# Kernel optimization log

Hardware: AMD Instinct MI355X
Metric: run time of the kernel (lower is better)

The kernel has to match this reference:

```python
import jax, jax.numpy as jnp
import numpy as np

EMBED_DIM = 1024
NUM_HEADS = 16
HEAD_DIM = EMBED_DIM // NUM_HEADS


def setup_inputs() -> dict:
    key = jax.random.key(0)
    ks = jax.random.split(key, 6)
    B, S, D = 2, 2048, EMBED_DIM
    scale = 1.0 / np.sqrt(D)
    return {
        "inputs": jax.random.normal(ks[0], (B, S, D), dtype=jnp.float32),
        "Wq": jax.random.normal(ks[1], (D, D), dtype=jnp.float32) * scale,
        "Wk": jax.random.normal(ks[2], (D, D), dtype=jnp.float32) * scale,
        "Wv": jax.random.normal(ks[3], (D, D), dtype=jnp.float32) * scale,
        "Wo": jax.random.normal(ks[4], (D, D), dtype=jnp.float32) * scale,
        "bo": jnp.zeros((D,), dtype=jnp.float32),
    }


def reference(inputs, Wq, Wk, Wv, Wo, bo):
    B, S, D = inputs.shape
    H, P = NUM_HEADS, HEAD_DIM
    # torch Linear: x @ W.T ; weights stored [out, in]
    q = inputs @ Wq.T
    k = inputs @ Wk.T
    v = inputs @ Wv.T
    # separate heads: [B, S, H, P] -> [B, H, S, P]
    q = q.reshape(B, S, H, P).transpose(0, 2, 1, 3)
    k = k.reshape(B, S, H, P).transpose(0, 2, 1, 3)
    v = v.reshape(B, S, H, P).transpose(0, 2, 1, 3)
    # scaled dot-product attention; scale = 1/sqrt(P + 1e-9)
    scale = 1.0 / jnp.sqrt(jnp.float32(P) + 1e-9)
    scores = jnp.einsum("bhsp,bhtp->bhst", q, k) * scale
    weights = jax.nn.softmax(scores, axis=-1)
    attn = jnp.einsum("bhst,bhtp->bhsp", weights, v)
    # merge heads -> [B, S, D]
    concat = attn.transpose(0, 2, 1, 3).reshape(B, S, D)
    return concat @ Wo.T + bo
```

## Files before the change

### kernel.cpp

```cpp
#include <hip/hip_runtime.h>
#include <hip/hip_bf16.h>

typedef __bf16 bf16;
typedef __bf16 bf16x4 __attribute__((ext_vector_type(4)));
typedef __bf16 bf16x8 __attribute__((ext_vector_type(8)));
typedef short  s16x4  __attribute__((ext_vector_type(4)));
typedef float  f32x4  __attribute__((ext_vector_type(4)));

#define QSCALE 0.18033688011112042f

__device__ __forceinline__ void load16_lds(const bf16* g, bf16* l) {
    __builtin_amdgcn_global_load_lds(
        (const __attribute__((address_space(1))) unsigned int*)g,
        (__attribute__((address_space(3))) unsigned int*)l, 16, 0, 0);
}

__global__ void cvt_f32_bf16(
    const float* __restrict__ s0, const float* __restrict__ s1,
    const float* __restrict__ s2, const float* __restrict__ s3,
    const float* __restrict__ s4,
    bf16* __restrict__ d0, bf16* __restrict__ d1, bf16* __restrict__ d2,
    bf16* __restrict__ d3, bf16* __restrict__ d4)
{
    const float* s; bf16* d; int nblk;
    switch (blockIdx.y) {
        case 0:  s = s0; d = d0; nblk = 2048; break;
        case 1:  s = s1; d = d1; nblk = 512;  break;
        case 2:  s = s2; d = d2; nblk = 512;  break;
        case 3:  s = s3; d = d3; nblk = 512;  break;
        default: s = s4; d = d4; nblk = 512;  break;
    }
    if ((int)blockIdx.x >= nblk) return;
    int idx = blockIdx.x * 256 + threadIdx.x;
    float4 a = ((const float4*)s)[idx * 2];
    float4 b = ((const float4*)s)[idx * 2 + 1];
    bf16x8 o;
    o[0] = (bf16)a.x; o[1] = (bf16)a.y; o[2] = (bf16)a.z; o[3] = (bf16)a.w;
    o[4] = (bf16)b.x; o[5] = (bf16)b.y; o[6] = (bf16)b.z; o[7] = (bf16)b.w;
    *(bf16x8*)&d[idx * 8] = o;
}

__global__ __launch_bounds__(256, 2) void qkv_gemm(
    const bf16* __restrict__ A,
    const bf16* __restrict__ Wq, const bf16* __restrict__ Wk,
    const bf16* __restrict__ Wv,
    bf16* __restrict__ qbuf, bf16* __restrict__ kbuf, bf16* __restrict__ vT)
{
    __shared__ bf16 sA[128 * 32];
    __shared__ bf16 sB[128 * 32];

    const int which = blockIdx.x >> 3;
    const int n0    = (blockIdx.x & 7) * 128;
    const int m0    = blockIdx.y * 128;
    const bf16* B   = (which == 0) ? Wq : (which == 1) ? Wk : Wv;

    const int tid  = threadIdx.x;
    const int lane = tid & 63;
    const int w    = tid >> 6;
    const int wr   = w >> 1, wc = w & 1;
    const int r    = lane & 15;
    const int qd   = lane >> 4;

    f32x4 acc[4][4];
    const f32x4 zero4 = {0.f, 0.f, 0.f, 0.f};
#pragma unroll
    for (int mi = 0; mi < 4; ++mi)
#pragma unroll
        for (int ni = 0; ni < 4; ++ni) acc[mi][ni] = zero4;

    for (int kt = 0; kt < 32; ++kt) {
        const bf16* gA = A + (size_t)m0 * 1024 + kt * 32;
        const bf16* gB = B + (size_t)n0 * 1024 + kt * 32;
        __syncthreads();
#pragma unroll
        for (int j = 0; j < 2; ++j) {
            int task = j * 256 + tid;
            int row  = task >> 2, ch = task & 3;
            int ldsb = (j * 256 + w * 64) * 8;
            load16_lds(gA + (size_t)row * 1024 + ch * 8, &sA[ldsb]);
            load16_lds(gB + (size_t)row * 1024 + ch * 8, &sB[ldsb]);
        }
        __syncthreads();

        bf16x8 af[4], bfr[4];
#pragma unroll
        for (int mi = 0; mi < 4; ++mi)
            af[mi] = *(const bf16x8*)&sA[(wr * 64 + mi * 16 + r) * 32 + qd * 8];
#pragma unroll
        for (int ni = 0; ni < 4; ++ni)
            bfr[ni] = *(const bf16x8*)&sB[(wc * 64 + ni * 16 + r) * 32 + qd * 8];
#pragma unroll
        for (int mi = 0; mi < 4; ++mi)
#pragma unroll
            for (int ni = 0; ni < 4; ++ni)
                acc[mi][ni] = __builtin_amdgcn_mfma_f32_16x16x32_bf16(
                    af[mi], bfr[ni], acc[mi][ni], 0, 0, 0);
    }

    const float scale = (which == 0) ? QSCALE : 1.0f;
#pragma unroll
    for (int mi = 0; mi < 4; ++mi)
#pragma unroll
        for (int ni = 0; ni < 4; ++ni)
#pragma unroll
            for (int i = 0; i < 4; ++i) {
                int row = m0 + wr * 64 + mi * 16 + qd * 4 + i;
                int col = n0 + wc * 64 + ni * 16 + r;
                float v = acc[mi][ni][i] * scale;
                if (which == 0) {
                    qbuf[(size_t)row * 1024 + col] = (bf16)v;
                } else if (which == 1) {
                    kbuf[(size_t)row * 1024 + col] = (bf16)v;
                } else {
                    vT[((size_t)((row >> 11) * 1024 + col)) * 2048 + (row & 2047)] = (bf16)v;
                }
            }
}

__global__ __launch_bounds__(256, 2) void out_gemm(
    const bf16* __restrict__ A, const bf16* __restrict__ B,
    float* __restrict__ C, const float* __restrict__ bias)
{
    __shared__ bf16 sA[128 * 32];
    __shared__ bf16 sB[64 * 32];

    const int tid  = threadIdx.x;
    const int lane = tid & 63;
    const int w    = tid >> 6;
    const int wr   = w >> 1, wc = w & 1;
    const int r    = lane & 15;
    const int qd   = lane >> 4;
    const int m0   = blockIdx.y * 128;
    const int n0   = blockIdx.x * 64;

    f32x4 acc[4][2];
    const f32x4 zero4 = {0.f, 0.f, 0.f, 0.f};
#pragma unroll
    for (int mi = 0; mi < 4; ++mi)
#pragma unroll
        for (int ni = 0; ni < 2; ++ni) acc[mi][ni] = zero4;

    for (int kt = 0; kt < 32; ++kt) {
        const bf16* gA = A + (size_t)m0 * 1024 + kt * 32;
        const bf16* gB = B + (size_t)n0 * 1024 + kt * 32;
        __syncthreads();
#pragma unroll
        for (int j = 0; j < 2; ++j) {
            int task = j * 256 + tid;
            int row  = task >> 2, ch = task & 3;
            int ldsb = (j * 256 + w * 64) * 8;
            load16_lds(gA + (size_t)row * 1024 + ch * 8, &sA[ldsb]);
        }
        {
            int row = tid >> 2, ch = tid & 3;
            int ldsb = (w * 64) * 8;
            load16_lds(gB + (size_t)row * 1024 + ch * 8, &sB[ldsb]);
        }
        __syncthreads();

        bf16x8 af[4], bfr[2];
#pragma unroll
        for (int mi = 0; mi < 4; ++mi)
            af[mi] = *(const bf16x8*)&sA[(wr * 64 + mi * 16 + r) * 32 + qd * 8];
#pragma unroll
        for (int ni = 0; ni < 2; ++ni)
            bfr[ni] = *(const bf16x8*)&sB[(wc * 32 + ni * 16 + r) * 32 + qd * 8];
#pragma unroll
        for (int mi = 0; mi < 4; ++mi)
#pragma unroll
            for (int ni = 0; ni < 2; ++ni)
                acc[mi][ni] = __builtin_amdgcn_mfma_f32_16x16x32_bf16(
                    af[mi], bfr[ni], acc[mi][ni], 0, 0, 0);
    }

#pragma unroll
    for (int mi = 0; mi < 4; ++mi)
#pragma unroll
        for (int ni = 0; ni < 2; ++ni)
#pragma unroll
            for (int i = 0; i < 4; ++i) {
                int row = m0 + wr * 64 + mi * 16 + qd * 4 + i;
                int col = n0 + wc * 32 + ni * 16 + r;
                C[(size_t)row * 1024 + col] = acc[mi][ni][i] + bias[col];
            }
}

__global__ __launch_bounds__(256, 2) void attn_kernel(
    const bf16* __restrict__ qbuf, const bf16* __restrict__ kbuf,
    const bf16* __restrict__ vT, bf16* __restrict__ concat)
{
    __shared__ bf16 sKV[4 * 64 * 72];

    const int tid  = threadIdx.x;
    const int lane = tid & 63;
    const int w    = tid >> 6;
    const int r    = lane & 15;
    const int qd   = lane >> 4;
    const int qt   = blockIdx.x;
    const int bh   = blockIdx.y;
    const int b    = bh >> 4, h = bh & 15;
    const int qrow0 = b * 2048 + qt * 128;
    const size_t vbase = (size_t)bh * 64 * 2048;

    const s16x4 ones4 = {(short)0x3F80, (short)0x3F80, (short)0x3F80, (short)0x3F80};

    int krow[2], kch[2];
#pragma unroll
    for (int t = 0; t < 2; ++t) {
        int flat = t * 256 + tid;
        krow[t] = flat >> 3; kch[t] = flat & 7;
    }

    bf16x8 aq[2][2];
#pragma unroll
    for (int mi = 0; mi < 2; ++mi)
#pragma unroll
        for (int ks = 0; ks < 2; ++ks)
            aq[mi][ks] = *(const bf16x8*)&qbuf[
                (size_t)(qrow0 + w * 32 + mi * 16 + r) * 1024 + h * 64 + ks * 32 + qd * 8];

    f32x4 acc_o[2][4], acc_l[2];
    const f32x4 zero4 = {0.f, 0.f, 0.f, 0.f};
#pragma unroll
    for (int mi = 0; mi < 2; ++mi) {
        acc_l[mi] = zero4;
#pragma unroll
        for (int pj = 0; pj < 4; ++pj) acc_o[mi][pj] = zero4;
    }

    bf16x8 rk[2], rv[2];
#pragma unroll
    for (int t = 0; t < 2; ++t) {
        rk[t] = *(const bf16x8*)&kbuf[(size_t)(b * 2048 + krow[t]) * 1024 + h * 64 + kch[t] * 8];
        rv[t] = *(const bf16x8*)&vT[vbase + (size_t)krow[t] * 2048 + kch[t] * 8];
    }
#pragma unroll
    for (int t = 0; t < 2; ++t) {
        *(bf16x8*)&sKV[0 * 4608 + krow[t] * 72 + kch[t] * 8] = rk[t];
        *(bf16x8*)&sKV[1 * 4608 + krow[t] * 72 + kch[t] * 8] = rv[t];
    }
#pragma unroll
    for (int t = 0; t < 2; ++t) {
        rk[t] = *(const bf16x8*)&kbuf[(size_t)(b * 2048 + 64 + krow[t]) * 1024 + h * 64 + kch[t] * 8];
        rv[t] = *(const bf16x8*)&vT[vbase + (size_t)krow[t] * 2048 + 64 + kch[t] * 8];
    }
    __syncthreads();

    for (int tt = 0; tt < 32; ++tt) {
        {
            int st = (tt + 1) & 1;
#pragma unroll
            for (int t = 0; t < 2; ++t) {
                *(bf16x8*)&sKV[(2 * st + 0) * 4608 + krow[t] * 72 + kch[t] * 8] = rk[t];
                *(bf16x8*)&sKV[(2 * st + 1) * 4608 + krow[t] * 72 + kch[t] * 8] = rv[t];
            }
        }
        {
            int nxt = (tt + 2 < 32) ? tt + 2 : 31;
#pragma unroll
            for (int t = 0; t < 2; ++t) {
                rk[t] = *(const bf16x8*)&kbuf[(size_t)(b * 2048 + nxt * 64 + krow[t]) * 1024 + h * 64 + kch[t] * 8];
                rv[t] = *(const bf16x8*)&vT[vbase + (size_t)krow[t] * 2048 + nxt * 64 + kch[t] * 8];
            }
        }
        const bf16* sK = &sKV[(2 * (tt & 1) + 0) * 4608];
        const bf16* sV = &sKV[(2 * (tt & 1) + 1) * 4608];

        f32x4 accs[2][4];
#pragma unroll
        for (int mi = 0; mi < 2; ++mi)
#pragma unroll
            for (int ni = 0; ni < 4; ++ni) accs[mi][ni] = zero4;
#pragma unroll
        for (int ks = 0; ks < 2; ++ks)
#pragma unroll
            for (int ni = 0; ni < 4; ++ni) {
                bf16x8 ak = *(const bf16x8*)&sK[(ni * 16 + r) * 72 + ks * 32 + qd * 8];
#pragma unroll
                for (int mi = 0; mi < 2; ++mi)
                    accs[mi][ni] = __builtin_amdgcn_mfma_f32_16x16x32_bf16(
                        ak, aq[mi][ks], accs[mi][ni], 0, 0, 0);
            }

        s16x4 pfrag[2][4];
#pragma unroll
        for (int mi = 0; mi < 2; ++mi)
#pragma unroll
            for (int ni = 0; ni < 4; ++ni) {
                bf16x4 pv;
#pragma unroll
                for (int i = 0; i < 4; ++i) pv[i] = (bf16)exp2f(accs[mi][ni][i]);
                pfrag[mi][ni] = __builtin_bit_cast(s16x4, pv);
            }

#pragma unroll
        for (int ni = 0; ni < 4; ++ni) {
#pragma unroll
            for (int pj = 0; pj < 4; ++pj) {
                bf16x4 av = *(const bf16x4*)&sV[(pj * 16 + r) * 72 + ni * 16 + qd * 4];
                s16x4  avs = __builtin_bit_cast(s16x4, av);
#pragma unroll
                for (int mi = 0; mi < 2; ++mi)
                    acc_o[mi][pj] = __builtin_amdgcn_mfma_f32_16x16x16bf16_1k(
                        avs, pfrag[mi][ni], acc_o[mi][pj], 0, 0, 0);
            }
#pragma unroll
            for (int mi = 0; mi < 2; ++mi)
                acc_l[mi] = __builtin_amdgcn_mfma_f32_16x16x16bf16_1k(
                    ones4, pfrag[mi][ni], acc_l[mi], 0, 0, 0);
        }

        __syncthreads();
    }

    bf16* scratch = sKV;
#pragma unroll
    for (int mi = 0; mi < 2; ++mi) {
        float inv = 1.0f / acc_l[mi][0];
        int qloc  = w * 32 + mi * 16 + r;
#pragma unroll
        for (int pj = 0; pj < 4; ++pj)
#pragma unroll
            for (int i = 0; i < 4; ++i)
                scratch[qloc * 72 + pj * 16 + qd * 4 + i] =
                    (bf16)(acc_o[mi][pj][i] * inv);
    }
    __syncthreads();
    {
        int row  = tid >> 1;
        int half = tid & 1;
#pragma unroll
        for (int c = 0; c < 4; ++c) {
            bf16x8 v = *(const bf16x8*)&scratch[row * 72 + half * 32 + c * 8];
            *(bf16x8*)&concat[(size_t)(qrow0 + row) * 1024 + h * 64 + half * 32 + c * 8] = v;
        }
    }
}

extern "C" void kernel_launch(void* const* d_in, const int* in_sizes, int n_in,
                              void* d_out, int out_size, void* d_ws, size_t ws_size,
                              hipStream_t stream)
{
    const float* x  = (const float*)d_in[0];
    const float* Wq = (const float*)d_in[1];
    const float* Wk = (const float*)d_in[2];
    const float* Wv = (const float*)d_in[3];
    const float* Wo = (const float*)d_in[4];
    const float* bo = (const float*)d_in[5];
    float* out = (float*)d_out;

    char* ws = (char*)d_ws;
    bf16* xb     = (bf16*)(ws);
    bf16* Wqb    = (bf16*)(ws + (8u  << 20));
    bf16* Wkb    = (bf16*)(ws + (10u << 20));
    bf16* Wvb    = (bf16*)(ws + (12u << 20));
    bf16* Wob    = (bf16*)(ws + (14u << 20));
    bf16* qbuf   = (bf16*)(ws + (16u << 20));
    bf16* kbuf   = (bf16*)(ws + (24u << 20));
    bf16* vT     = (bf16*)(ws + (32u << 20));
    bf16* concat = (bf16*)(ws + (40u << 20));

    hipLaunchKernelGGL(cvt_f32_bf16, dim3(2048, 5), dim3(256), 0, stream,
                       x, Wq, Wk, Wv, Wo, xb, Wqb, Wkb, Wvb, Wob);
    hipLaunchKernelGGL(qkv_gemm, dim3(24, 32), dim3(256), 0, stream,
                       xb, Wqb, Wkb, Wvb, qbuf, kbuf, vT);
    hipLaunchKernelGGL(attn_kernel, dim3(16, 32), dim3(256), 0, stream,
                       qbuf, kbuf, vT, concat);
    hipLaunchKernelGGL(out_gemm, dim3(16, 32), dim3(256), 0, stream,
                       concat, Wob, out, bo);
}
```

Measured before the change: 206.3 us.

## Split attention KV sequence across two wave groups and vectorize V-transpose stores

The attention kernel now runs 512 threads per block as two groups of four waves. Each group handles alternating 64-key tiles for the same 128 queries, using its own double-buffered LDS region, and the partial O and row-sum accumulators are merged through LDS at the end. This doubles the waves working per query tile to raise latency hiding and occupancy, at the cost of more LDS, a reduction step and a larger register budget per block. Separately, the QKV GEMM epilogue writes the transposed V as packed 4-element bf16 vectors instead of scalar stores.

```diff
diff --git a/kernel.cpp b/kernel.cpp
--- a/kernel.cpp
+++ b/kernel.cpp
@@ -101,20 +101,21 @@
 #pragma unroll
     for (int mi = 0; mi < 4; ++mi)
 #pragma unroll
-        for (int ni = 0; ni < 4; ++ni)
-#pragma unroll
-            for (int i = 0; i < 4; ++i) {
-                int row = m0 + wr * 64 + mi * 16 + qd * 4 + i;
-                int col = n0 + wc * 64 + ni * 16 + r;
-                float v = acc[mi][ni][i] * scale;
-                if (which == 0) {
-                    qbuf[(size_t)row * 1024 + col] = (bf16)v;
-                } else if (which == 1) {
-                    kbuf[(size_t)row * 1024 + col] = (bf16)v;
-                } else {
-                    vT[((size_t)((row >> 11) * 1024 + col)) * 2048 + (row & 2047)] = (bf16)v;
-                }
-            }
+        for (int ni = 0; ni < 4; ++ni) {
+            int rb  = m0 + wr * 64 + mi * 16 + qd * 4;
+            int col = n0 + wc * 64 + ni * 16 + r;
+            if (which == 2) {
+                bf16x4 pv;
+#pragma unroll
+                for (int i = 0; i < 4; ++i) pv[i] = (bf16)acc[mi][ni][i];
+                *(bf16x4*)&vT[((size_t)((rb >> 11) * 1024 + col)) * 2048 + (rb & 2047)] = pv;
+            } else {
+                bf16* dst = (which == 0) ? qbuf : kbuf;
+#pragma unroll
+                for (int i = 0; i < 4; ++i)
+                    dst[(size_t)(rb + i) * 1024 + col] = (bf16)(acc[mi][ni][i] * scale);
+            }
+        }
 }
 
 __global__ __launch_bounds__(256, 2) void out_gemm(
@@ -185,15 +186,18 @@
             }
 }
 
-__global__ __launch_bounds__(256, 2) void attn_kernel(
+__global__ __launch_bounds__(512, 4) void attn_kernel(
     const bf16* __restrict__ qbuf, const bf16* __restrict__ kbuf,
     const bf16* __restrict__ vT, bf16* __restrict__ concat)
 {
-    __shared__ bf16 sKV[4 * 64 * 72];
+    __shared__ bf16 sKV[8 * 64 * 72];
 
     const int tid  = threadIdx.x;
     const int lane = tid & 63;
     const int w    = tid >> 6;
+    const int g    = w >> 2;
+    const int wq   = w & 3;
+    const int gtid = tid & 255;
     const int r    = lane & 15;
     const int qd   = lane >> 4;
     const int qt   = blockIdx.x;
@@ -207,7 +211,7 @@
     int krow[2], kch[2];
 #pragma unroll
     for (int t = 0; t < 2; ++t) {
-        int flat = t * 256 + tid;
+        int flat = t * 256 + gtid;
         krow[t] = flat >> 3; kch[t] = flat & 7;
     }
 
@@ -217,7 +221,7 @@
 #pragma unroll
         for (int ks = 0; ks < 2; ++ks)
             aq[mi][ks] = *(const bf16x8*)&qbuf[
-                (size_t)(qrow0 + w * 32 + mi * 16 + r) * 1024 + h * 64 + ks * 32 + qd * 8];
+                (size_t)(qrow0 + wq * 32 + mi * 16 + r) * 1024 + h * 64 + ks * 32 + qd * 8];
 
     f32x4 acc_o[2][4], acc_l[2];
     const f32x4 zero4 = {0.f, 0.f, 0.f, 0.f};
@@ -228,43 +232,46 @@
         for (int pj = 0; pj < 4; ++pj) acc_o[mi][pj] = zero4;
     }
 
+    bf16* const myKV = &sKV[g * 4 * 4608];
+
     bf16x8 rk[2], rv[2];
 #pragma unroll
     for (int t = 0; t < 2; ++t) {
-        rk[t] = *(const bf16x8*)&kbuf[(size_t)(b * 2048 + krow[t]) * 1024 + h * 64 + kch[t] * 8];
-        rv[t] = *(const bf16x8*)&vT[vbase + (size_t)krow[t] * 2048 + kch[t] * 8];
+        rk[t] = *(const bf16x8*)&kbuf[(size_t)(b * 2048 + g * 64 + krow[t]) * 1024 + h * 64 + kch[t] * 8];
+        rv[t] = *(const bf16x8*)&vT[vbase + (size_t)krow[t] * 2048 + g * 64 + kch[t] * 8];
     }
 #pragma unroll
     for (int t = 0; t < 2; ++t) {
-        *(bf16x8*)&sKV[0 * 4608 + krow[t] * 72 + kch[t] * 8] = rk[t];
-        *(bf16x8*)&sKV[1 * 4608 + krow[t] * 72 + kch[t] * 8] = rv[t];
+        *(bf16x8*)&myKV[0 * 4608 + krow[t] * 72 + kch[t] * 8] = rk[t];
+        *(bf16x8*)&myKV[1 * 4608 + krow[t] * 72 + kch[t] * 8] = rv[t];
     }
 #pragma unroll
     for (int t = 0; t < 2; ++t) {
-        rk[t] = *(const bf16x8*)&kbuf[(size_t)(b * 2048 + 64 + krow[t]) * 1024 + h * 64 + kch[t] * 8];
-        rv[t] = *(const bf16x8*)&vT[vbase + (size_t)krow[t] * 2048 + 64 + kch[t] * 8];
+        rk[t] = *(const bf16x8*)&kbuf[(size_t)(b * 2048 + (2 + g) * 64 + krow[t]) * 1024 + h * 64 + kch[t] * 8];
+        rv[t] = *(const bf16x8*)&vT[vbase + (size_t)krow[t] * 2048 + (2 + g) * 64 + kch[t] * 8];
     }
     __syncthreads();
 
-    for (int tt = 0; tt < 32; ++tt) {
+    for (int tt = 0; tt < 16; ++tt) {
         {
             int st = (tt + 1) & 1;
 #pragma unroll
             for (int t = 0; t < 2; ++t) {
-                *(bf16x8*)&sKV[(2 * st + 0) * 4608 + krow[t] * 72 + kch[t] * 8] = rk[t];
-                *(bf16x8*)&sKV[(2 * st + 1) * 4608 + krow[t] * 72 + kch[t] * 8] = rv[t];
+                *(bf16x8*)&myKV[(2 * st + 0) * 4608 + krow[t] * 72 + kch[t] * 8] = rk[t];
+                *(bf16x8*)&myKV[(2 * st + 1) * 4608 + krow[t] * 72 + kch[t] * 8] = rv[t];
             }
         }
         {
-            int nxt = (tt + 2 < 32) ? tt + 2 : 31;
+            int nxtl = (tt + 2 < 16) ? tt + 2 : 15;
+            int gt   = 2 * nxtl + g;
 #pragma unroll
             for (int t = 0; t < 2; ++t) {
-                rk[t] = *(const bf16x8*)&kbuf[(size_t)(b * 2048 + nxt * 64 + krow[t]) * 1024 + h * 64 + kch[t] * 8];
-                rv[t] = *(const bf16x8*)&vT[vbase + (size_t)krow[t] * 2048 + nxt * 64 + kch[t] * 8];
-            }
-        }
-        const bf16* sK = &sKV[(2 * (tt & 1) + 0) * 4608];
-        const bf16* sV = &sKV[(2 * (tt & 1) + 1) * 4608];
+                rk[t] = *(const bf16x8*)&kbuf[(size_t)(b * 2048 + gt * 64 + krow[t]) * 1024 + h * 64 + kch[t] * 8];
+                rv[t] = *(const bf16x8*)&vT[vbase + (size_t)krow[t] * 2048 + gt * 64 + kch[t] * 8];
+            }
+        }
+        const bf16* sK = &myKV[(2 * (tt & 1) + 0) * 4608];
+        const bf16* sV = &myKV[(2 * (tt & 1) + 1) * 4608];
 
         f32x4 accs[2][4];
 #pragma unroll
@@ -313,27 +320,47 @@
         __syncthreads();
     }
 
-    bf16* scratch = sKV;
-#pragma unroll
-    for (int mi = 0; mi < 2; ++mi) {
-        float inv = 1.0f / acc_l[mi][0];
-        int qloc  = w * 32 + mi * 16 + r;
-#pragma unroll
-        for (int pj = 0; pj < 4; ++pj)
-#pragma unroll
-            for (int i = 0; i < 4; ++i)
-                scratch[qloc * 72 + pj * 16 + qd * 4 + i] =
-                    (bf16)(acc_o[mi][pj][i] * inv);
+    float* sF = (float*)sKV;
+    bf16*  sO = sKV + 18432;
+
+    if (g == 1) {
+        int slot = gtid * 35;
+#pragma unroll
+        for (int mi = 0; mi < 2; ++mi)
+#pragma unroll
+            for (int pj = 0; pj < 4; ++pj)
+#pragma unroll
+                for (int i = 0; i < 4; ++i)
+                    sF[slot + mi * 16 + pj * 4 + i] = acc_o[mi][pj][i];
+        sF[slot + 32] = acc_l[0][0];
+        sF[slot + 33] = acc_l[1][0];
+    }
+    __syncthreads();
+    if (g == 0) {
+        int slot = gtid * 35;
+        float inv[2];
+#pragma unroll
+        for (int mi = 0; mi < 2; ++mi)
+            inv[mi] = 1.0f / (acc_l[mi][0] + sF[slot + 32 + mi]);
+#pragma unroll
+        for (int mi = 0; mi < 2; ++mi) {
+            int qloc = wq * 32 + mi * 16 + r;
+#pragma unroll
+            for (int pj = 0; pj < 4; ++pj)
+#pragma unroll
+                for (int i = 0; i < 4; ++i) {
+                    float o = acc_o[mi][pj][i] + sF[slot + mi * 16 + pj * 4 + i];
+                    sO[qloc * 72 + pj * 16 + qd * 4 + i] = (bf16)(o * inv[mi]);
+                }
+        }
     }
     __syncthreads();
     {
-        int row  = tid >> 1;
-        int half = tid & 1;
-#pragma unroll
-        for (int c = 0; c < 4; ++c) {
-            bf16x8 v = *(const bf16x8*)&scratch[row * 72 + half * 32 + c * 8];
-            *(bf16x8*)&concat[(size_t)(qrow0 + row) * 1024 + h * 64 + half * 32 + c * 8] = v;
-        }
+        int row = tid >> 2;
+        int q4  = tid & 3;
+        size_t cb = (size_t)(qrow0 + row) * 1024 + h * 64 + q4 * 16;
+        *(bf16x8*)&concat[cb]     = *(const bf16x8*)&sO[row * 72 + q4 * 16];
+        *(bf16x8*)&concat[cb + 8] = *(const bf16x8*)&sO[row * 72 + q4 * 16 + 8];
     }
 }
 
@@ -364,7 +391,7 @@
                        x, Wq, Wk, Wv, Wo, xb, Wqb, Wkb, Wvb, Wob);
     hipLaunchKernelGGL(qkv_gemm, dim3(24, 32), dim3(256), 0, stream,
                        xb, Wqb, Wkb, Wvb, qbuf, kbuf, vT);
-    hipLaunchKernelGGL(attn_kernel, dim3(16, 32), dim3(256), 0, stream,
+    hipLaunchKernelGGL(attn_kernel, dim3(16, 32), dim3(512), 0, stream,
                        qbuf, kbuf, vT, concat);
     hipLaunchKernelGGL(out_gemm, dim3(16, 32), dim3(256), 0, stream,
                        concat, Wob, out, bo);
```

Result: faster. 195.8 us (-5.1%).
